# Kernel tuning notes

Measured on AMD Instinct MI355X. Metric: run time of the kernel, lower is better.

## Reference

```python
import jax, jax.numpy as jnp
import numpy as np

B_, L_, DM = 8, 1024, 256
DS, DC, EX = 16, 4, 2
DI = EX * DM            # d_inner = 512
DTR = max(1, DM // 16)  # dt_rank = 16


def setup_inputs() -> dict:
    key = jax.random.key(0)
    ks = iter(jax.random.split(key, 40))
    def n(shape, s=0.02):
        return jax.random.normal(next(ks), shape, jnp.float32) * s
    inp = {"x": jax.random.normal(next(ks), (B_, L_, DM), jnp.float32)}
    inp["norm_g"] = jnp.ones((DM,), jnp.float32)
    inp["norm_b"] = jnp.zeros((DM,), jnp.float32)
    for m in ("f", "b"):
        inp[f"inW_{m}"] = n((DM, 2 * DI))
        inp[f"convW_{m}"] = n((DI, DC))
        inp[f"convB_{m}"] = jnp.zeros((DI,), jnp.float32)
        inp[f"xW_{m}"] = n((DI, DTR + 2 * DS))
        inp[f"dtW_{m}"] = n((DTR, DI))
        inp[f"dtB_{m}"] = jnp.zeros((DI,), jnp.float32)
        # ALog init: log of [1..dState] repeated over dInner rows
        inp[f"ALog_{m}"] = jnp.log(jnp.tile(jnp.arange(1, DS + 1, dtype=jnp.float32), (DI, 1)))
        inp[f"Dp_{m}"] = jnp.ones((DI,), jnp.float32)
        inp[f"outW_{m}"] = n((DI, DM))
    inp["fusW"] = n((2 * DM, DM))
    inp["fusB"] = jnp.zeros((DM,), jnp.float32)
    return inp


def _dw_conv(x, w, b):
    # causal depthwise conv1d: x [B,L,DI], w [DI,DC] -> [B,L,DI]
    xc = jnp.transpose(x, (0, 2, 1))  # B,DI,L
    out = jax.lax.conv_general_dilated(
        xc, w[:, None, :], window_strides=(1,), padding=[(DC - 1, 0)],
        dimension_numbers=("NCH", "OIH", "NCH"), feature_group_count=DI)
    return jnp.transpose(out + b[:, None], (0, 2, 1))


def _ssm(x, xW, dtW, dtB, ALog, Dp):
    # x: [B,L,DI]
    A = -jnp.exp(ALog)                                   # [DI,DS]
    xdbl = x @ xW                                        # [B,L,DTR+2*DS]
    dlt, Bp, Cp = jnp.split(xdbl, [DTR, DTR + DS], axis=-1)
    delta = jax.nn.softplus(dlt @ dtW + dtB)             # [B,L,DI]
    dA = jnp.exp(delta[..., None] * A)                   # [B,L,DI,DS]
    dBx = (delta * x)[..., None] * Bp[:, :, None, :]     # [B,L,DI,DS]

    def step(h, t):
        a, bb, c = t
        h = a * h + bb                                   # [B,DI,DS]
        y = jnp.einsum('bdn,bn->bd', h, c)
        return h, y

    h0 = jnp.zeros((x.shape[0], DI, DS), x.dtype)
    _, ys = jax.lax.scan(step, h0, (jnp.moveaxis(dA, 1, 0),
                                    jnp.moveaxis(dBx, 1, 0),
                                    jnp.moveaxis(Cp, 1, 0)))
    return jnp.moveaxis(ys, 0, 1) + Dp * x               # [B,L,DI]


def _mamba(x, inW, convW, convB, xW, dtW, dtB, ALog, Dp, outW):
    xr = x @ inW                                         # [B,L,2*DI]
    xs, res = jnp.split(xr, 2, axis=-1)
    xs = jax.nn.silu(_dw_conv(xs, convW, convB))
    y = _ssm(xs, xW, dtW, dtB, ALog, Dp)
    return (y * jax.nn.silu(res)) @ outW                 # [B,L,DM]


def reference(x, norm_g, norm_b,
              inW_f, convW_f, convB_f, xW_f, dtW_f, dtB_f, ALog_f, Dp_f, outW_f,
              inW_b, convW_b, convB_b, xW_b, dtW_b, dtB_b, ALog_b, Dp_b, outW_b,
              fusW, fusB):
    # LayerNorm
    mu = x.mean(-1, keepdims=True)
    var = ((x - mu) ** 2).mean(-1, keepdims=True)
    xn = (x - mu) * jax.lax.rsqrt(var + 1e-5) * norm_g + norm_b
    # forward-direction Mamba
    xf = _mamba(xn, inW_f, convW_f, convB_f, xW_f, dtW_f, dtB_f, ALog_f, Dp_f, outW_f)
    # backward-direction Mamba (flip along time)
    xb = _mamba(jnp.flip(xn, 1), inW_b, convW_b, convB_b, xW_b, dtW_b, dtB_b, ALog_b, Dp_b, outW_b)
    xb = jnp.flip(xb, 1)
    fused = jnp.concatenate([xf, xb], axis=-1) @ fusW + fusB
    return x + fused  # dropout is identity in eval
```

## Files before the change

### kernel.cpp

```cpp
#include <hip/hip_runtime.h>
#include <cmath>

typedef __bf16 bf16x8 __attribute__((ext_vector_type(8)));
typedef __bf16 bf16x4 __attribute__((ext_vector_type(4)));
typedef float  f32x4  __attribute__((ext_vector_type(4)));
typedef float  f32x2  __attribute__((ext_vector_type(2)));

#define B_  8
#define L_  1024
#define DM  256
#define DI  512
#define DS  16
#define DTR 16
#define M_  (B_*L_)
#define NC  32
#define CT  32

__device__ inline float softplus_f(float z){
  return (z > 20.f) ? z : __logf(1.f + __expf(z));
}
__device__ inline float silu_f(float z){
  return z / (1.f + __expf(-z));
}

__device__ inline int flag_from_x(const void* x){
  const unsigned short* u = (const unsigned short*)x;
  int lane = threadIdx.x & 63;
  unsigned short v = u[2*lane];
  int e = (v >> 7) & 0xFF;
  unsigned long long m = __ballot(e >= 160 || e < 96);
  return __popcll(m) > 16;
}

struct PrepJob { const void* src; void* dst; int rows; int cols; int f32out; };
struct PrepArgs { PrepJob j[26]; int nj; };
struct TJob { const void* src; __bf16* dst; int R; int C; };
struct TArgs { TJob j[3]; int ntiles[3]; int nj; int ntot; };

__global__ __launch_bounds__(256) void wprep_k(TArgs ta, PrepArgs a, const void* xsrc){
  const int f = flag_from_x(xsrc);
  const int tid = threadIdx.x;
  if ((int)blockIdx.x < ta.ntot){
    __shared__ float tile[64][65];
    int bid = blockIdx.x;
    int jj = 0;
    while (jj < ta.nj-1 && bid >= ta.ntiles[jj]) { bid -= ta.ntiles[jj]; jj++; }
    const TJob J = ta.j[jj];
    const int tpr = J.C >> 6;
    const int tr = bid / tpr, tc = bid - tr*tpr;
    const int r0 = tr*64, c0 = tc*64;
    #pragma unroll
    for (int i=0;i<16;i++){
      int idx = i*256 + tid;
      int r = idx >> 6, c = idx & 63;
      long off = (long)(r0+r)*J.C + c0 + c;
      tile[r][c] = f ? ((const float*)J.src)[off] : (float)((const __bf16*)J.src)[off];
    }
    __syncthreads();
    #pragma unroll
    for (int i=0;i<16;i++){
      int idx = i*256 + tid;
      int c = idx >> 6, r = idx & 63;
      J.dst[(long)(c0+c)*J.R + r0 + r] = (__bf16)tile[r][c];
    }
  } else {
    int e = (blockIdx.x - ta.ntot)*256 + tid;
    #pragma unroll 1
    for (int jj=0; jj<a.nj; jj++){
      int sz = a.j[jj].rows * a.j[jj].cols;
      if (e < sz){
        int cols = a.j[jj].cols;
        int r = e / cols, c = e - r*cols;
        float v = f ? ((const float*)a.j[jj].src)[e] : (float)((const __bf16*)a.j[jj].src)[e];
        if (a.j[jj].f32out) ((float*)a.j[jj].dst)[c*a.j[jj].rows + r] = v;
        else ((__bf16*)a.j[jj].dst)[(long)c*a.j[jj].rows + r] = (__bf16)v;
        return;
      }
      e -= sz;
    }
  }
}

__global__ __launch_bounds__(256) void lnw_k(
    const void* x, const __bf16* g, const __bf16* bb, __bf16* xn,
    const __bf16* fusWt, const __bf16* outWr0, const __bf16* outWr1,
    __bf16* BtC0, __bf16* BtC1)
{
  const int bx = blockIdx.x;
  const int tid = threadIdx.x;
  const int lane = tid & 63;
  const int wid = tid >> 6;

  if (bx < M_/4){
    const int f = flag_from_x(x);
    long row = (long)bx*4 + wid;
    long base = row*DM + lane*4;
    float v0,v1,v2,v3;
    if (f){ f32x4 xv = *(const f32x4*)((const float*)x + base);
            v0=xv[0]; v1=xv[1]; v2=xv[2]; v3=xv[3]; }
    else  { bf16x4 xv = *(const bf16x4*)((const __bf16*)x + base);
            v0=(float)xv[0]; v1=(float)xv[1]; v2=(float)xv[2]; v3=(float)xv[3]; }
    float s = v0+v1+v2+v3;
    float q = v0*v0+v1*v1+v2*v2+v3*v3;
    #pragma unroll
    for (int off=32; off>0; off>>=1){ s += __shfl_xor(s,off); q += __shfl_xor(q,off); }
    float mu = s*(1.f/DM), var = q*(1.f/DM)-mu*mu;
    float rs = rsqrtf(var+1e-5f);
    bf16x4 gv = *(const bf16x4*)(g + lane*4);
    bf16x4 bv = *(const bf16x4*)(bb + lane*4);
    bf16x4 o;
    o[0]=(__bf16)((v0-mu)*rs*(float)gv[0]+(float)bv[0]);
    o[1]=(__bf16)((v1-mu)*rs*(float)gv[1]+(float)bv[1]);
    o[2]=(__bf16)((v2-mu)*rs*(float)gv[2]+(float)bv[2]);
    o[3]=(__bf16)((v3-mu)*rs*(float)gv[3]+(float)bv[3]);
    *(bf16x4*)(xn + base) = o;
  } else {
    int b2 = bx - M_/4;
    int wz  = b2 >> 5;
    int rem = b2 & 31;
    int gx = rem & 3, gy = rem >> 2;
    const __bf16* A  = fusWt + wz*DM;
    const __bf16* Bt = wz ? outWr1 : outWr0;
    __bf16* C = wz ? BtC1 : BtC0;
    const int mBase = (gx*4 + wid)*16;
    const int nBase = gy*64;
    const int lm = lane & 15;
    const int kq = (lane >> 4)*8;
    long aoff = (long)(mBase+lm)*(2*DM) + kq;
    long boff[4];
    #pragma unroll
    for (int j=0;j<4;j++) boff[j] = (long)(nBase+j*16+lm)*DM + kq;
    f32x4 acc[4] = {};
    #pragma unroll
    for (int k0=0;k0<DM;k0+=32){
      bf16x8 af = *(const bf16x8*)(A + aoff + k0);
      bf16x8 bfr[4];
      #pragma unroll
      for (int j=0;j<4;j++) bfr[j] = *(const bf16x8*)(Bt + boff[j] + k0);
      #pragma unroll
      for (int j=0;j<4;j++)
        acc[j] = __builtin_amdgcn_mfma_f32_16x16x32_bf16(af, bfr[j], acc[j], 0,0,0);
    }
    #pragma unroll
    for (int rr=0;rr<4;rr++){
      int r = mBase + (lane>>4)*4 + rr;
      #pragma unroll
      for (int j=0;j<4;j++){
        int c = nBase + j*16 + lm;
        C[(long)r*DI + c] = (__bf16)acc[j][rr];
      }
    }
  }
}

template<int BM,int BN,int KK>
__global__ __launch_bounds__(256) void gemm_in_k(
    const __bf16* A, const __bf16* B0, const __bf16* B1,
    __bf16* xz0, __bf16* xz1, __bf16* res0, __bf16* res1,
    int lda, int ldb)
{
  constexpr int TM = BM/2, TN = BN/2;
  constexpr int WMT = TM/16, WNT = TN/16;
  constexpr int LA = BM/64, LB = BN/64;

  const int dir = blockIdx.z;
  const __bf16* Bt = dir ? B1 : B0;
  __bf16* xz  = dir ? xz1 : xz0;
  __bf16* res = dir ? res1 : res0;
  const int tid  = threadIdx.x;
  const int lane = tid & 63;
  const int wid  = tid >> 6;
  const int wm = wid & 1;
  const int wn = wid >> 1;
  const int mBase = blockIdx.x * BM;
  const int nBase = blockIdx.y * BN;
  const int lm = lane & 15;
  const int kq = (lane >> 4) * 8;

  __shared__ __bf16 As[BM*32];
  __shared__ __bf16 Bs[BN*32];

  const __bf16* aS[LA];
  const __bf16* bS[LB];
  {
    int colk = (tid & 3) * 8;
    #pragma unroll
    for (int ld=0; ld<LA; ld++){
      int r = mBase + ld*64 + (tid >> 2);
      if (dir==1){ int b = r >> 10, t = r & (L_-1); r = (b<<10) + (L_-1-t); }
      aS[ld] = A + (long)r*lda + colk;
    }
    #pragma unroll
    for (int ld=0; ld<LB; ld++){
      int r = nBase + ld*64 + (tid >> 2);
      bS[ld] = Bt + (long)r*ldb + colk;
    }
  }

  f32x4 acc[WMT][WNT] = {};
  for (int k0=0; k0<KK; k0+=32){
    #pragma unroll
    for (int ld=0; ld<LA; ld++)
      __builtin_amdgcn_global_load_lds(
        (const __attribute__((address_space(1))) void*)(aS[ld] + k0),
        (__attribute__((address_space(3))) void*)(&As[ld*2048 + tid*8]), 16, 0, 0);
    #pragma unroll
    for (int ld=0; ld<LB; ld++)
      __builtin_amdgcn_global_load_lds(
        (const __attribute__((address_space(1))) void*)(bS[ld] + k0),
        (__attribute__((address_space(3))) void*)(&Bs[ld*2048 + tid*8]), 16, 0, 0);
    __syncthreads();
    bf16x8 af[WMT], bfr[WNT];
    #pragma unroll
    for (int i=0;i<WMT;i++) af[i]  = *(const bf16x8*)&As[(wm*TM + i*16 + lm)*32 + kq];
    #pragma unroll
    for (int j=0;j<WNT;j++) bfr[j] = *(const bf16x8*)&Bs[(wn*TN + j*16 + lm)*32 + kq];
    #pragma unroll
    for (int i=0;i<WMT;i++)
      #pragma unroll
      for (int j=0;j<WNT;j++)
        acc[i][j] = __builtin_amdgcn_mfma_f32_16x16x32_bf16(af[i], bfr[j], acc[i][j], 0,0,0);
    __syncthreads();
  }

  #pragma unroll
  for (int i=0;i<WMT;i++){
    #pragma unroll
    for (int rr=0;rr<4;rr++){
      int r = mBase + wm*TM + i*16 + (lane>>4)*4 + rr;
      #pragma unroll
      for (int j=0;j<WNT;j++){
        int c = nBase + wn*TN + j*16 + lm;
        float v = acc[i][j][rr];
        if (c < DI) xz[(long)r*DI + c] = (__bf16)v;
        else        res[(long)r*DI + (c-DI)] = (__bf16)v;
      }
    }
  }
}

template<int BM,int BN,int KK>
__global__ __launch_bounds__(256) void gemm_fin_k(
    const __bf16* Af, const __bf16* Ab,
    const __bf16* Bt0, const __bf16* Bt1,
    void* Cout, const __bf16* bias, const void* resid)
{
  constexpr int TM = BM/2, TN = BN/2;
  constexpr int WMT = TM/16, WNT = TN/16;
  constexpr int LA = BM/64, LB = BN/64;

  const int of = flag_from_x(resid);
  const int tid  = threadIdx.x;
  const int lane = tid & 63;
  const int wid  = tid >> 6;
  const int wm = wid & 1;
  const int wn = wid >> 1;
  const int mBase = blockIdx.x * BM;
  const int nBase = blockIdx.y * BN;
  const int lm = lane & 15;
  const int kq = (lane >> 4) * 8;

  __shared__ __bf16 As[BM*32];
  __shared__ __bf16 Bs[BN*32];

  f32x4 acc[WMT][WNT] = {};
  #pragma unroll 1
  for (int dd=0; dd<2; dd++){
    const __bf16* A  = dd ? Ab  : Af;
    const __bf16* Bt = dd ? Bt1 : Bt0;
    const __bf16* aS[LA];
    const __bf16* bS[LB];
    {
      int colk = (tid & 3) * 8;
      #pragma unroll
      for (int ld=0; ld<LA; ld++){
        int r = mBase + ld*64 + (tid >> 2);
        if (dd==1){ int b = r >> 10, t = r & (L_-1); r = (b<<10) + (L_-1-t); }
        aS[ld] = A + (long)r*DI + colk;
      }
      #pragma unroll
      for (int ld=0; ld<LB; ld++){
        int r = nBase + ld*64 + (tid >> 2);
        bS[ld] = Bt + (long)r*DI + colk;
      }
    }
    for (int k0=0; k0<KK; k0+=32){
      #pragma unroll
      for (int ld=0; ld<LA; ld++)
        __builtin_amdgcn_global_load_lds(
          (const __attribute__((address_space(1))) void*)(aS[ld] + k0),
          (__attribute__((address_space(3))) void*)(&As[ld*2048 + tid*8]), 16, 0, 0);
      #pragma unroll
      for (int ld=0; ld<LB; ld++)
        __builtin_amdgcn_global_load_lds(
          (const __attribute__((address_space(1))) void*)(bS[ld] + k0),
          (__attribute__((address_space(3))) void*)(&Bs[ld*2048 + tid*8]), 16, 0, 0);
      __syncthreads();
      bf16x8 af[WMT], bfr[WNT];
      #pragma unroll
      for (int i=0;i<WMT;i++) af[i]  = *(const bf16x8*)&As[(wm*TM + i*16 + lm)*32 + kq];
      #pragma unroll
      for (int j=0;j<WNT;j++) bfr[j] = *(const bf16x8*)&Bs[(wn*TN + j*16 + lm)*32 + kq];
      #pragma unroll
      for (int i=0;i<WMT;i++)
        #pragma unroll
        for (int j=0;j<WNT;j++)
          acc[i][j] = __builtin_amdgcn_mfma_f32_16x16x32_bf16(af[i], bfr[j], acc[i][j], 0,0,0);
      __syncthreads();
    }
  }

  #pragma unroll
  for (int i=0;i<WMT;i++){
    #pragma unroll
    for (int rr=0;rr<4;rr++){
      int r = mBase + wm*TM + i*16 + (lane>>4)*4 + rr;
      #pragma unroll
      for (int j=0;j<WNT;j++){
        int c = nBase + wn*TN + j*16 + lm;
        float v = acc[i][j][rr];
        float rsd = of ? ((const float*)resid)[(long)r*DM + c]
                       : (float)((const __bf16*)resid)[(long)r*DM + c];
        v += (float)bias[c] + rsd;
        if (of) ((float*)Cout)[(long)r*DM + c] = v;
        else    ((__bf16*)Cout)[(long)r*DM + c] = (__bf16)v;
      }
    }
  }
}

__global__ __launch_bounds__(512) void scanA_k(
    const __bf16* xz0, const __bf16* xz1,
    const float* cw0, const float* cw1,
    const __bf16* cb0, const __bf16* cb1,
    const __bf16* xW0, const __bf16* xW1,
    const float* dw0, const float* dw1,
    const __bf16* dtB0, const __bf16* dtB1,
    const float* ALf0, const float* ALf1,
    float* hend, float* sumd)
{
  const int dir = blockIdx.z;
  const __bf16* xz  = dir ? xz1 : xz0;
  const float*  cw  = dir ? cw1 : cw0;
  const __bf16* cb  = dir ? cb1 : cb0;
  const __bf16* xWt = dir ? xW1 : xW0;
  const float*  dw  = dir ? dw1 : dw0;
  const __bf16* dtB = dir ? dtB1 : dtB0;
  const float*  ALf = dir ? ALf1 : ALf0;

  const int b   = blockIdx.y;
  const int c   = blockIdx.x;
  const int tid = threadIdx.x;
  const int lane = tid & 63;
  const int wid  = tid >> 6;
  const int d   = tid;
  const int db  = dir*8 + b;
  const long row0 = (long)b*L_ + c*CT;

  __shared__ __bf16 xs_s[CT*DI];
  __shared__ float  sX[CT][48];

  {
    const float c0 = cw[0*DI+d], c1 = cw[1*DI+d], c2 = cw[2*DI+d], c3 = cw[3*DI+d];
    const float cbv = (float)cb[d];
    int gt0 = c*CT;
    float xm3 = (gt0-3 >= 0) ? (float)xz[(row0-3)*DI + d] : 0.f;
    float xm2 = (gt0-2 >= 0) ? (float)xz[(row0-2)*DI + d] : 0.f;
    float xm1 = (gt0-1 >= 0) ? (float)xz[(row0-1)*DI + d] : 0.f;
    #pragma unroll 8
    for (int t=0;t<CT;t++){
      float xt = (float)xz[(row0+t)*DI + d];
      float a = cbv;
      a += xm3*c0; a += xm2*c1; a += xm1*c2; a += xt*c3;
      float sv = silu_f(a);
      *(__bf16*)((char*)xs_s + t*1024 + ((2*d) ^ ((t&7)<<4))) = (__bf16)sv;
      xm3 = xm2; xm2 = xm1; xm1 = xt;
    }
  }
  __syncthreads();

  if (wid < 6){
    const int mb = (wid & 1) * 16;
    const int nb = (wid >> 1) * 16;
    const int lm = lane & 15;
    const int kq = (lane >> 4) * 8;
    const int row = mb + lm;
    const char* abase = (const char*)xs_s + row*1024;
    const int rsw = (row&7)<<4;
    const __bf16* Bt = xWt + (long)(nb + lm)*DI + kq;
    f32x4 acc = {};
    #pragma unroll
    for (int k0=0;k0<DI;k0+=32){
      bf16x8 af  = *(const bf16x8*)(abase + (((kq + k0)*2) ^ rsw));
      bf16x8 bfr = *(const bf16x8*)(Bt + k0);
      acc = __builtin_amdgcn_mfma_f32_16x16x32_bf16(af, bfr, acc, 0,0,0);
    }
    #pragma unroll
    for (int rr=0;rr<4;rr++){
      int r = mb + (lane>>4)*4 + rr;
      sX[r][nb + lm] = acc[rr];
    }
  }

  f32x2 dw2[8];
  { const f32x4* p = (const f32x4*)(dw + d*DTR);
    #pragma unroll
    for (int q=0;q<4;q++){ f32x4 v=p[q];
      dw2[q*2]   = f32x2{v[0],v[1]};
      dw2[q*2+1] = f32x2{v[2],v[3]}; } }
  float A[16];
  { const f32x4* p = (const f32x4*)(ALf + d*DS);
    #pragma unroll
    for (int q=0;q<4;q++){ f32x4 v=p[q];
      A[q*4]=-__expf(v[0]); A[q*4+1]=-__expf(v[1]); A[q*4+2]=-__expf(v[2]); A[q*4+3]=-__expf(v[3]); } }
  bool pow_ok = true;
  #pragma unroll
  for (int n=0;n<16;n++) pow_ok = pow_ok && (fabsf(A[n] + (float)(n+1)) < 0.003f*(n+1));
  const float dtbv = (float)dtB[d];

  f32x2 h2[8];
  #pragma unroll
  for (int i=0;i<8;i++) h2[i] = f32x2{0.f,0.f};
  float sdelta = 0.f;
  __syncthreads();

  if (pow_ok){
    #pragma unroll 2
    for (int t=0;t<CT;t++){
      f32x2 z2 = f32x2{dtbv, 0.f};
      #pragma unroll
      for (int i=0;i<8;i++){
        f32x2 qv = *(const f32x2*)&sX[t][i*2];
        z2 += qv*dw2[i];
      }
      float delta = softplus_f(z2[0]+z2[1]);
      sdelta += delta;
      float xv = (float)*(const __bf16*)((const char*)xs_s + t*1024 + ((2*d) ^ ((t&7)<<4)));
      float dx = delta*xv;
      f32x2 dx2 = f32x2{dx, dx};
      float e1 = __expf(-delta), e2v = e1*e1;
      f32x2 e22 = f32x2{e2v, e2v};
      f32x2 pw = f32x2{e1, e2v};
      #pragma unroll
      for (int i=0;i<8;i++){
        f32x2 Bv = *(const f32x2*)&sX[t][16+i*2];
        h2[i] = pw*h2[i] + dx2*Bv;
        pw = pw*e22;
      }
    }
  } else {
    #pragma unroll 2
    for (int t=0;t<CT;t++){
      f32x2 z2 = f32x2{dtbv, 0.f};
      #pragma unroll
      for (int i=0;i<8;i++){
        f32x2 qv = *(const f32x2*)&sX[t][i*2];
        z2 += qv*dw2[i];
      }
      float delta = softplus_f(z2[0]+z2[1]);
      sdelta += delta;
      float xv = (float)*(const __bf16*)((const char*)xs_s + t*1024 + ((2*d) ^ ((t&7)<<4)));
      float dx = delta*xv;
      #pragma unroll
      for (int i=0;i<8;i++){
        f32x2 Bv = *(const f32x2*)&sX[t][16+i*2];
        f32x2 pw = f32x2{__expf(delta*A[i*2]), __expf(delta*A[i*2+1])};
        h2[i] = pw*h2[i] + f32x2{dx,dx}*Bv;
      }
    }
  }

  long hb = (((long)db*NC + c)*DI + d)*16;
  f32x4* hp = (f32x4*)(hend + hb);
  #pragma unroll
  for (int q=0;q<4;q++){
    f32x4 v; v[0]=h2[q*2][0]; v[1]=h2[q*2][1]; v[2]=h2[q*2+1][0]; v[3]=h2[q*2+1][1];
    hp[q]=v;
  }
  sumd[((long)db*NC + c)*DI + d] = sdelta;
}

__global__ __launch_bounds__(256) void scanB_k(
    const float* ALf0, const float* ALf1,
    const float* hend, const float* sumd, float* Hbuf)
{
  int gid = blockIdx.x*256 + threadIdx.x;
  int n  = gid & 15;
  int d  = (gid>>4) & 511;
  int db = gid >> 13;
  const float* ALf = (db>=8) ? ALf1 : ALf0;
  float A_dn = -__expf(ALf[d*DS + n]);
  const long base0 = (((long)db*NC)*DI + d)*16 + n;
  const long cstr  = (long)DI*16;
  const long sbase = (long)db*NC*DI + d;
  float he[NC], Sv[NC];
  #pragma unroll
  for (int c=0;c<NC;c++) he[c] = hend[base0 + c*cstr];
  #pragma unroll
  for (int c=0;c<NC;c++) Sv[c] = sumd[sbase + c*DI];
  float H = 0.f;
  #pragma unroll
  for (int c=0;c<NC;c++){
    Hbuf[base0 + c*cstr] = H;
    H = he[c] + __expf(A_dn*Sv[c])*H;
  }
}

__global__ __launch_bounds__(512) void scanC_k(
    const __bf16* xz0, const __bf16* xz1,
    const float* cw0, const float* cw1,
    const __bf16* cb0, const __bf16* cb1,
    const __bf16* xW0, const __bf16* xW1,
    __bf16* res0, __bf16* res1,
    const float* dw0, const float* dw1,
    const __bf16* dtB0, const __bf16* dtB1,
    const float* ALf0, const float* ALf1,
    const __bf16* Dp0, const __bf16* Dp1,
    const float* Hbuf)
{
  const int dir = blockIdx.z;
  const __bf16* xz  = dir ? xz1 : xz0;
  const float*  cw  = dir ? cw1 : cw0;
  const __bf16* cb  = dir ? cb1 : cb0;
  const __bf16* xWt = dir ? xW1 : xW0;
  __bf16*       res = dir ? res1 : res0;
  const float*  dw  = dir ? dw1 : dw0;
  const __bf16* dtB = dir ? dtB1 : dtB0;
  const float*  ALf = dir ? ALf1 : ALf0;
  const __bf16* Dp  = dir ? Dp1 : Dp0;

  const int b   = blockIdx.y;
  const int c   = blockIdx.x;
  const int tid = threadIdx.x;
  const int lane = tid & 63;
  const int wid  = tid >> 6;
  const int d   = tid;
  const int db  = dir*8 + b;
  const long row0 = (long)b*L_ + c*CT;

  __shared__ __bf16 xs_s[CT*DI];
  __shared__ float  sX[CT][48];

  {
    const float c0 = cw[0*DI+d], c1 = cw[1*DI+d], c2 = cw[2*DI+d], c3 = cw[3*DI+d];
    const float cbv = (float)cb[d];
    int gt0 = c*CT;
    float xm3 = (gt0-3 >= 0) ? (float)xz[(row0-3)*DI + d] : 0.f;
    float xm2 = (gt0-2 >= 0) ? (float)xz[(row0-2)*DI + d] : 0.f;
    float xm1 = (gt0-1 >= 0) ? (float)xz[(row0-1)*DI + d] : 0.f;
    #pragma unroll 8
    for (int t=0;t<CT;t++){
      float xt = (float)xz[(row0+t)*DI + d];
      float a = cbv;
      a += xm3*c0; a += xm2*c1; a += xm1*c2; a += xt*c3;
      float sv = silu_f(a);
      *(__bf16*)((char*)xs_s + t*1024 + ((2*d) ^ ((t&7)<<4))) = (__bf16)sv;
      xm3 = xm2; xm2 = xm1; xm1 = xt;
    }
  }
  __syncthreads();

  if (wid < 6){
    const int mb = (wid & 1) * 16;
    const int nb = (wid >> 1) * 16;
    const int lm = lane & 15;
    const int kq = (lane >> 4) * 8;
    const int row = mb + lm;
    const char* abase = (const char*)xs_s + row*1024;
    const int rsw = (row&7)<<4;
    const __bf16* Bt = xWt + (long)(nb + lm)*DI + kq;
    f32x4 acc = {};
    #pragma unroll
    for (int k0=0;k0<DI;k0+=32){
      bf16x8 af  = *(const bf16x8*)(abase + (((kq + k0)*2) ^ rsw));
      bf16x8 bfr = *(const bf16x8*)(Bt + k0);
      acc = __builtin_amdgcn_mfma_f32_16x16x32_bf16(af, bfr, acc, 0,0,0);
    }
    #pragma unroll
    for (int rr=0;rr<4;rr++){
      int r = mb + (lane>>4)*4 + rr;
      sX[r][nb + lm] = acc[rr];
    }
  }

  f32x2 dw2[8];
  { const f32x4* p = (const f32x4*)(dw + d*DTR);
    #pragma unroll
    for (int q=0;q<4;q++){ f32x4 v=p[q];
      dw2[q*2]   = f32x2{v[0],v[1]};
      dw2[q*2+1] = f32x2{v[2],v[3]}; } }
  float A[16];
  { const f32x4* p = (const f32x4*)(ALf + d*DS);
    #pragma unroll
    for (int q=0;q<4;q++){ f32x4 v=p[q];
      A[q*4]=-__expf(v[0]); A[q*4+1]=-__expf(v[1]); A[q*4+2]=-__expf(v[2]); A[q*4+3]=-__expf(v[3]); } }
  bool pow_ok = true;
  #pragma unroll
  for (int n=0;n<16;n++) pow_ok = pow_ok && (fabsf(A[n] + (float)(n+1)) < 0.003f*(n+1));
  const float dtbv = (float)dtB[d];

  f32x2 h2[8];
  { long hb = (((long)db*NC + c)*DI + d)*16;
    const f32x4* p = (const f32x4*)(Hbuf + hb);
    #pragma unroll
    for (int q=0;q<4;q++){ f32x4 v = p[q];
      h2[q*2]   = f32x2{v[0],v[1]};
      h2[q*2+1] = f32x2{v[2],v[3]}; } }
  const float Dpv = (float)Dp[d];
  __syncthreads();

  if (pow_ok){
    #pragma unroll 2
    for (int t=0;t<CT;t++){
      long row = row0 + t;
      f32x2 z2 = f32x2{dtbv, 0.f};
      #pragma unroll
      for (int i=0;i<8;i++){
        f32x2 qv = *(const f32x2*)&sX[t][i*2];
        z2 += qv*dw2[i];
      }
      float delta = softplus_f(z2[0]+z2[1]);
      float xv = (float)*(const __bf16*)((const char*)xs_s + t*1024 + ((2*d) ^ ((t&7)<<4)));
      float dx = delta*xv;
      f32x2 dx2 = f32x2{dx, dx};
      float e1 = __expf(-delta), e2v = e1*e1;
      f32x2 e22 = f32x2{e2v, e2v};
      f32x2 pw = f32x2{e1, e2v};
      f32x2 p2 = f32x2{0.f, 0.f};
      #pragma unroll
      for (int i=0;i<8;i++){
        f32x2 Bv = *(const f32x2*)&sX[t][16+i*2];
        f32x2 Cv = *(const f32x2*)&sX[t][32+i*2];
        h2[i] = pw*h2[i] + dx2*Bv;
        p2 += h2[i]*Cv;
        pw = pw*e22;
      }
      float yv = p2[0] + p2[1] + Dpv*xv;
      float rv = (float)res[row*DI + d];
      res[row*DI + d] = (__bf16)(yv * silu_f(rv));
    }
  } else {
    #pragma unroll 2
    for (int t=0;t<CT;t++){
      long row = row0 + t;
      f32x2 z2 = f32x2{dtbv, 0.f};
      #pragma unroll
      for (int i=0;i<8;i++){
        f32x2 qv = *(const f32x2*)&sX[t][i*2];
        z2 += qv*dw2[i];
      }
      float delta = softplus_f(z2[0]+z2[1]);
      float xv = (float)*(const __bf16*)((const char*)xs_s + t*1024 + ((2*d) ^ ((t&7)<<4)));
      float dx = delta*xv;
      f32x2 p2 = f32x2{0.f, 0.f};
      #pragma unroll
      for (int i=0;i<8;i++){
        f32x2 Bv = *(const f32x2*)&sX[t][16+i*2];
        f32x2 Cv = *(const f32x2*)&sX[t][32+i*2];
        f32x2 pw = f32x2{__expf(delta*A[i*2]), __expf(delta*A[i*2+1])};
        h2[i] = pw*h2[i] + f32x2{dx,dx}*Bv;
        p2 += h2[i]*Cv;
      }
      float yv = p2[0] + p2[1] + Dpv*xv;
      float rv = (float)res[row*DI + d];
      res[row*DI + d] = (__bf16)(yv * silu_f(rv));
    }
  }
}

extern "C" void kernel_launch(void* const* d_in, const int* in_sizes, int n_in,
                              void* d_out, int out_size, void* d_ws, size_t ws_size,
                              hipStream_t stream)
{
  const size_t MB = 1u<<20;
  if (ws_size < 160*MB) return;

  char* w = (char*)d_ws;
  __bf16* xz[2]  = {(__bf16*)(w + 0),      (__bf16*)(w + 8*MB)};
  __bf16* res[2] = {(__bf16*)(w + 16*MB),  (__bf16*)(w + 24*MB)};
  __bf16* xn     = (__bf16*)(w + 48*MB);

  char* wp = w + 52*MB;
  auto carve = [&](size_t bytes)->void*{
    void* p = wp;
    wp += (bytes + 255) & ~(size_t)255;
    return p;
  };
  __bf16 *inWt[2], *xWt[2], *outWr[2], *BtC[2];
  float *dtWt[2], *convWt[2];
  for (int m=0;m<2;m++){
    inWt[m]   = (__bf16*)carve((size_t)(2*DI)*DM*2);
    xWt[m]    = (__bf16*)carve((size_t)48*DI*2);
    outWr[m]  = (__bf16*)carve((size_t)DI*DM*2);
    BtC[m]    = (__bf16*)carve((size_t)DM*DI*2);
    dtWt[m]   = (float*)carve((size_t)DI*DTR*4);
    convWt[m] = (float*)carve((size_t)4*DI*4);
  }
  __bf16* fusWt = (__bf16*)carve((size_t)DM*(2*DM)*2);
  float* ALf[2] = {(float*)carve((size_t)DI*DS*4), (float*)carve((size_t)DI*DS*4)};

  char* cp = w + 57*MB;
  auto carve2 = [&](size_t elems)->__bf16*{
    __bf16* p = (__bf16*)cp;
    cp += (elems*2 + 255) & ~(size_t)255;
    return p;
  };
  __bf16* ngc = carve2(DM);
  __bf16* nbc = carve2(DM);
  __bf16 *convBc[2], *dtBc[2], *Dpc[2];
  for (int m=0;m<2;m++){
    convBc[m] = carve2(DI);
    dtBc[m]   = carve2(DI);
    Dpc[m]    = carve2(DI);
  }
  __bf16* fusBc = carve2(DM);

  float* hend = (float*)(w + 90*MB);
  float* sumd = (float*)(w + 124*MB);
  float* Hbuf = (float*)(w + 127*MB);

  PrepArgs pa;
  int ji = 0;
  size_t tot = 0;
  auto addj = [&](const void* s, void* dst, int rows, int cols, int f32o){
    pa.j[ji++] = {s, dst, rows, cols, f32o};
    tot += (size_t)rows*cols;
  };
  for (int m=0;m<2;m++){
    int base = 3 + m*9;
    addj(d_in[base+3], xWt[m],   DI,  48,   0);
    addj(d_in[base+8], outWr[m], 1,   DI*DM,0);
    addj(d_in[base+4], dtWt[m],  DTR, DI,   1);
    addj(d_in[base+1], convWt[m],DI,  4,    1);
    addj(d_in[base+2], convBc[m],1, DI, 0);
    addj(d_in[base+5], dtBc[m],  1, DI, 0);
    addj(d_in[base+6], (void*)ALf[m], 1, DI*DS, 1);
    addj(d_in[base+7], Dpc[m],   1, DI, 0);
  }
  addj(d_in[1],  ngc, 1, DM, 0);
  addj(d_in[2],  nbc, 1, DM, 0);
  addj(d_in[22], fusBc, 1, DM, 0);
  pa.nj = ji;

  TArgs ta;
  ta.j[0] = { d_in[3],  inWt[0], DM,   2*DI }; ta.ntiles[0] = (DM/64)*((2*DI)/64);
  ta.j[1] = { d_in[12], inWt[1], DM,   2*DI }; ta.ntiles[1] = (DM/64)*((2*DI)/64);
  ta.j[2] = { d_in[21], fusWt,   2*DM, DM   }; ta.ntiles[2] = ((2*DM)/64)*(DM/64);
  ta.nj = 3;
  ta.ntot = ta.ntiles[0]+ta.ntiles[1]+ta.ntiles[2];
  int prepBlocks = (int)((tot+255)/256);
  wprep_k<<<ta.ntot + prepBlocks, 256, 0, stream>>>(ta, pa, d_in[0]);

  lnw_k<<<M_/4 + 64, 256, 0, stream>>>(
      d_in[0], ngc, nbc, xn, fusWt, outWr[0], outWr[1], BtC[0], BtC[1]);

  gemm_in_k<128,128,256><<<dim3(M_/128, (2*DI)/128, 2), 256, 0, stream>>>(
      xn, inWt[0], inWt[1], xz[0], xz[1], res[0], res[1], DM, DM);

  scanA_k<<<dim3(NC, B_, 2), 512, 0, stream>>>(
      xz[0], xz[1], convWt[0], convWt[1], convBc[0], convBc[1],
      xWt[0], xWt[1], dtWt[0], dtWt[1],
      dtBc[0], dtBc[1], ALf[0], ALf[1], hend, sumd);
  scanB_k<<<131072/256, 256, 0, stream>>>(ALf[0], ALf[1], hend, sumd, Hbuf);
  scanC_k<<<dim3(NC, B_, 2), 512, 0, stream>>>(
      xz[0], xz[1], convWt[0], convWt[1], convBc[0], convBc[1],
      xWt[0], xWt[1], res[0], res[1],
      dtWt[0], dtWt[1], dtBc[0], dtBc[1], ALf[0], ALf[1], Dpc[0], Dpc[1], Hbuf);

  gemm_fin_k<64,64,DI><<<dim3(M_/64, DM/64, 1), 256, 0, stream>>>(
      res[0], res[1], BtC[0], BtC[1], d_out, fusBc, d_in[0]);
}
```

Before: 236.4 us.

## Halve scan chunk length to double chunk count and trim per-thread registers

The time chunk size drops from 32 to 16 steps, so there are 64 chunks per sequence. This doubles the number of blocks in the chunked scan kernels and halves each block's serial recurrence. The MFMA projection tiles are reduced to a single 16-row tile. The per-thread A array is dropped and recomputed from ALog inside the fallback paths, which saves registers. In exchange, the cross-chunk carry kernel now runs a sequential chain twice as long, processed in groups of 16 to bound registers, and more carry state is written to workspace, so the buffers are moved.

```diff
diff --git a/kernel.cpp b/kernel.cpp
--- a/kernel.cpp
+++ b/kernel.cpp
@@ -13,8 +13,8 @@
 #define DS  16
 #define DTR 16
 #define M_  (B_*L_)
-#define NC  32
-#define CT  32
+#define NC  64
+#define CT  16
 
 __device__ inline float softplus_f(float z){
   return (z > 20.f) ? z : __logf(1.f + __expf(z));
@@ -358,7 +358,7 @@
   const long row0 = (long)b*L_ + c*CT;
 
   __shared__ __bf16 xs_s[CT*DI];
-  __shared__ float  sX[CT][48];
+  __shared__ float  sX[CT][32];
 
   {
     const float c0 = cw[0*DI+d], c1 = cw[1*DI+d], c2 = cw[2*DI+d], c3 = cw[3*DI+d];
@@ -367,7 +367,7 @@
     float xm3 = (gt0-3 >= 0) ? (float)xz[(row0-3)*DI + d] : 0.f;
     float xm2 = (gt0-2 >= 0) ? (float)xz[(row0-2)*DI + d] : 0.f;
     float xm1 = (gt0-1 >= 0) ? (float)xz[(row0-1)*DI + d] : 0.f;
-    #pragma unroll 8
+    #pragma unroll
     for (int t=0;t<CT;t++){
       float xt = (float)xz[(row0+t)*DI + d];
       float a = cbv;
@@ -379,12 +379,11 @@
   }
   __syncthreads();
 
-  if (wid < 6){
-    const int mb = (wid & 1) * 16;
-    const int nb = (wid >> 1) * 16;
+  if (wid < 2){
+    const int nb = wid * 16;
     const int lm = lane & 15;
     const int kq = (lane >> 4) * 8;
-    const int row = mb + lm;
+    const int row = lm;
     const char* abase = (const char*)xs_s + row*1024;
     const int rsw = (row&7)<<4;
     const __bf16* Bt = xWt + (long)(nb + lm)*DI + kq;
@@ -397,7 +396,7 @@
     }
     #pragma unroll
     for (int rr=0;rr<4;rr++){
-      int r = mb + (lane>>4)*4 + rr;
+      int r = (lane>>4)*4 + rr;
       sX[r][nb + lm] = acc[rr];
     }
   }
@@ -408,14 +407,12 @@
     for (int q=0;q<4;q++){ f32x4 v=p[q];
       dw2[q*2]   = f32x2{v[0],v[1]};
       dw2[q*2+1] = f32x2{v[2],v[3]}; } }
-  float A[16];
-  { const f32x4* p = (const f32x4*)(ALf + d*DS);
-    #pragma unroll
-    for (int q=0;q<4;q++){ f32x4 v=p[q];
-      A[q*4]=-__expf(v[0]); A[q*4+1]=-__expf(v[1]); A[q*4+2]=-__expf(v[2]); A[q*4+3]=-__expf(v[3]); } }
   bool pow_ok = true;
-  #pragma unroll
-  for (int n=0;n<16;n++) pow_ok = pow_ok && (fabsf(A[n] + (float)(n+1)) < 0.003f*(n+1));
+  #pragma unroll 1
+  for (int n=0;n<16;n++){
+    float An = -__expf(ALf[d*DS + n]);
+    pow_ok = pow_ok && (fabsf(An + (float)(n+1)) < 0.003f*(n+1));
+  }
   const float dtbv = (float)dtB[d];
 
   f32x2 h2[8];
@@ -463,8 +460,9 @@
       float dx = delta*xv;
       #pragma unroll
       for (int i=0;i<8;i++){
+        f32x2 A2 = f32x2{-__expf(ALf[d*DS+i*2]), -__expf(ALf[d*DS+i*2+1])};
         f32x2 Bv = *(const f32x2*)&sX[t][16+i*2];
-        f32x2 pw = f32x2{__expf(delta*A[i*2]), __expf(delta*A[i*2+1])};
+        f32x2 pw = f32x2{__expf(delta*A2[0]), __expf(delta*A2[1])};
         h2[i] = pw*h2[i] + f32x2{dx,dx}*Bv;
       }
     }
@@ -493,16 +491,20 @@
   const long base0 = (((long)db*NC)*DI + d)*16 + n;
   const long cstr  = (long)DI*16;
   const long sbase = (long)db*NC*DI + d;
-  float he[NC], Sv[NC];
-  #pragma unroll
-  for (int c=0;c<NC;c++) he[c] = hend[base0 + c*cstr];
-  #pragma unroll
-  for (int c=0;c<NC;c++) Sv[c] = sumd[sbase + c*DI];
   float H = 0.f;
-  #pragma unroll
-  for (int c=0;c<NC;c++){
-    Hbuf[base0 + c*cstr] = H;
-    H = he[c] + __expf(A_dn*Sv[c])*H;
+  #pragma unroll 1
+  for (int g=0; g<NC/16; g++){
+    float he[16], Sv[16];
+    #pragma unroll
+    for (int k=0;k<16;k++){
+      he[k] = hend[base0 + (long)(g*16+k)*cstr];
+      Sv[k] = sumd[sbase + (long)(g*16+k)*DI];
+    }
+    #pragma unroll
+    for (int k=0;k<16;k++){
+      Hbuf[base0 + (long)(g*16+k)*cstr] = H;
+      H = he[k] + __expf(A_dn*Sv[k])*H;
+    }
   }
 }
 
@@ -548,7 +550,7 @@
     float xm3 = (gt0-3 >= 0) ? (float)xz[(row0-3)*DI + d] : 0.f;
     float xm2 = (gt0-2 >= 0) ? (float)xz[(row0-2)*DI + d] : 0.f;
     float xm1 = (gt0-1 >= 0) ? (float)xz[(row0-1)*DI + d] : 0.f;
-    #pragma unroll 8
+    #pragma unroll
     for (int t=0;t<CT;t++){
       float xt = (float)xz[(row0+t)*DI + d];
       float a = cbv;
@@ -560,12 +562,11 @@
   }
   __syncthreads();
 
-  if (wid < 6){
-    const int mb = (wid & 1) * 16;
-    const int nb = (wid >> 1) * 16;
+  if (wid < 3){
+    const int nb = wid * 16;
     const int lm = lane & 15;
     const int kq = (lane >> 4) * 8;
-    const int row = mb + lm;
+    const int row = lm;
     const char* abase = (const char*)xs_s + row*1024;
     const int rsw = (row&7)<<4;
     const __bf16* Bt = xWt + (long)(nb + lm)*DI + kq;
@@ -578,7 +579,7 @@
     }
     #pragma unroll
     for (int rr=0;rr<4;rr++){
-      int r = mb + (lane>>4)*4 + rr;
+      int r = (lane>>4)*4 + rr;
       sX[r][nb + lm] = acc[rr];
     }
   }
@@ -589,14 +590,12 @@
     for (int q=0;q<4;q++){ f32x4 v=p[q];
       dw2[q*2]   = f32x2{v[0],v[1]};
       dw2[q*2+1] = f32x2{v[2],v[3]}; } }
-  float A[16];
-  { const f32x4* p = (const f32x4*)(ALf + d*DS);
-    #pragma unroll
-    for (int q=0;q<4;q++){ f32x4 v=p[q];
-      A[q*4]=-__expf(v[0]); A[q*4+1]=-__expf(v[1]); A[q*4+2]=-__expf(v[2]); A[q*4+3]=-__expf(v[3]); } }
   bool pow_ok = true;
-  #pragma unroll
-  for (int n=0;n<16;n++) pow_ok = pow_ok && (fabsf(A[n] + (float)(n+1)) < 0.003f*(n+1));
+  #pragma unroll 1
+  for (int n=0;n<16;n++){
+    float An = -__expf(ALf[d*DS + n]);
+    pow_ok = pow_ok && (fabsf(An + (float)(n+1)) < 0.003f*(n+1));
+  }
   const float dtbv = (float)dtB[d];
 
   f32x2 h2[8];
@@ -655,9 +654,10 @@
       f32x2 p2 = f32x2{0.f, 0.f};
       #pragma unroll
       for (int i=0;i<8;i++){
+        f32x2 A2 = f32x2{-__expf(ALf[d*DS+i*2]), -__expf(ALf[d*DS+i*2+1])};
         f32x2 Bv = *(const f32x2*)&sX[t][16+i*2];
         f32x2 Cv = *(const f32x2*)&sX[t][32+i*2];
-        f32x2 pw = f32x2{__expf(delta*A[i*2]), __expf(delta*A[i*2+1])};
+        f32x2 pw = f32x2{__expf(delta*A2[0]), __expf(delta*A2[1])};
         h2[i] = pw*h2[i] + f32x2{dx,dx}*Bv;
         p2 += h2[i]*Cv;
       }
@@ -716,8 +716,8 @@
   __bf16* fusBc = carve2(DM);
 
   float* hend = (float*)(w + 90*MB);
-  float* sumd = (float*)(w + 124*MB);
-  float* Hbuf = (float*)(w + 127*MB);
+  float* Hbuf = (float*)(w + 122*MB);
+  float* sumd = (float*)(w + 154*MB);
 
   PrepArgs pa;
   int ji = 0;
```

New measurement: 266.2 us. 1.13x slower.

## Halve scan chunk length and interleave two independent chunks per block

Applied to the files above, without the earlier changes.

The chunked selective scan now uses 64 chunks of 16 timesteps. Each block handles two adjacent chunks and runs their recurrences interleaved, so every thread carries two independent dependency chains, which halves the serial chain length and adds instruction-level parallelism. The first scan pass also skips computing the C projection it never used, leaving 4 MFMA waves instead of 6. In exchange the cross-chunk scanB pass handles twice as many chunk carries, the hend/Hbuf workspace doubles, and register pressure rises from holding two state vectors.

```diff
diff --git a/kernel.cpp b/kernel.cpp
--- a/kernel.cpp
+++ b/kernel.cpp
@@ -13,8 +13,9 @@
 #define DS  16
 #define DTR 16
 #define M_  (B_*L_)
-#define NC  32
-#define CT  32
+#define NC  64
+#define CT  16
+#define CTB 32
 
 __device__ inline float softplus_f(float z){
   return (z > 20.f) ? z : __logf(1.f + __expf(z));
@@ -349,29 +350,30 @@
   const float*  ALf = dir ? ALf1 : ALf0;
 
   const int b   = blockIdx.y;
-  const int c   = blockIdx.x;
+  const int g   = blockIdx.x;
+  const int c0  = g*2, c1 = g*2+1;
   const int tid = threadIdx.x;
   const int lane = tid & 63;
   const int wid  = tid >> 6;
   const int d   = tid;
   const int db  = dir*8 + b;
-  const long row0 = (long)b*L_ + c*CT;
-
-  __shared__ __bf16 xs_s[CT*DI];
-  __shared__ float  sX[CT][48];
+  const long row0 = (long)b*L_ + (long)c0*CT;
+
+  __shared__ __bf16 xs_s[CTB*DI];
+  __shared__ float  sX[CTB][32];
 
   {
-    const float c0 = cw[0*DI+d], c1 = cw[1*DI+d], c2 = cw[2*DI+d], c3 = cw[3*DI+d];
+    const float q0 = cw[0*DI+d], q1 = cw[1*DI+d], q2 = cw[2*DI+d], q3 = cw[3*DI+d];
     const float cbv = (float)cb[d];
-    int gt0 = c*CT;
+    int gt0 = c0*CT;
     float xm3 = (gt0-3 >= 0) ? (float)xz[(row0-3)*DI + d] : 0.f;
     float xm2 = (gt0-2 >= 0) ? (float)xz[(row0-2)*DI + d] : 0.f;
     float xm1 = (gt0-1 >= 0) ? (float)xz[(row0-1)*DI + d] : 0.f;
     #pragma unroll 8
-    for (int t=0;t<CT;t++){
+    for (int t=0;t<CTB;t++){
       float xt = (float)xz[(row0+t)*DI + d];
       float a = cbv;
-      a += xm3*c0; a += xm2*c1; a += xm1*c2; a += xt*c3;
+      a += xm3*q0; a += xm2*q1; a += xm1*q2; a += xt*q3;
       float sv = silu_f(a);
       *(__bf16*)((char*)xs_s + t*1024 + ((2*d) ^ ((t&7)<<4))) = (__bf16)sv;
       xm3 = xm2; xm2 = xm1; xm1 = xt;
@@ -379,7 +381,7 @@
   }
   __syncthreads();
 
-  if (wid < 6){
+  if (wid < 4){
     const int mb = (wid & 1) * 16;
     const int nb = (wid >> 1) * 16;
     const int lm = lane & 15;
@@ -418,66 +420,84 @@
   for (int n=0;n<16;n++) pow_ok = pow_ok && (fabsf(A[n] + (float)(n+1)) < 0.003f*(n+1));
   const float dtbv = (float)dtB[d];
 
-  f32x2 h2[8];
+  f32x2 hA[8], hB[8];
   #pragma unroll
-  for (int i=0;i<8;i++) h2[i] = f32x2{0.f,0.f};
-  float sdelta = 0.f;
+  for (int i=0;i<8;i++){ hA[i] = f32x2{0.f,0.f}; hB[i] = f32x2{0.f,0.f}; }
+  float sdA = 0.f, sdB = 0.f;
   __syncthreads();
 
   if (pow_ok){
     #pragma unroll 2
     for (int t=0;t<CT;t++){
-      f32x2 z2 = f32x2{dtbv, 0.f};
+      f32x2 zA = f32x2{dtbv, 0.f}, zB = f32x2{dtbv, 0.f};
       #pragma unroll
       for (int i=0;i<8;i++){
-        f32x2 qv = *(const f32x2*)&sX[t][i*2];
-        z2 += qv*dw2[i];
-      }
-      float delta = softplus_f(z2[0]+z2[1]);
-      sdelta += delta;
-      float xv = (float)*(const __bf16*)((const char*)xs_s + t*1024 + ((2*d) ^ ((t&7)<<4)));
-      float dx = delta*xv;
-      f32x2 dx2 = f32x2{dx, dx};
-      float e1 = __expf(-delta), e2v = e1*e1;
-      f32x2 e22 = f32x2{e2v, e2v};
-      f32x2 pw = f32x2{e1, e2v};
+        zA += (*(const f32x2*)&sX[t][i*2])      * dw2[i];
+        zB += (*(const f32x2*)&sX[CT+t][i*2])   * dw2[i];
+      }
+      float dlA = softplus_f(zA[0]+zA[1]);
+      float dlB = softplus_f(zB[0]+zB[1]);
+      sdA += dlA; sdB += dlB;
+      const int swz = (2*d) ^ ((t&7)<<4);
+      float xvA = (float)*(const __bf16*)((const char*)xs_s + t*1024 + swz);
+      float xvB = (float)*(const __bf16*)((const char*)xs_s + (CT+t)*1024 + swz);
+      float dxA = dlA*xvA, dxB = dlB*xvB;
+      float e1A = __expf(-dlA), e2A = e1A*e1A;
+      float e1B = __expf(-dlB), e2B = e1B*e1B;
+      f32x2 pwA = f32x2{e1A, e2A}, pwB = f32x2{e1B, e2B};
+      f32x2 e22A = f32x2{e2A, e2A}, e22B = f32x2{e2B, e2B};
       #pragma unroll
       for (int i=0;i<8;i++){
-        f32x2 Bv = *(const f32x2*)&sX[t][16+i*2];
-        h2[i] = pw*h2[i] + dx2*Bv;
-        pw = pw*e22;
+        f32x2 BvA = *(const f32x2*)&sX[t][16+i*2];
+        f32x2 BvB = *(const f32x2*)&sX[CT+t][16+i*2];
+        hA[i] = pwA*hA[i] + f32x2{dxA,dxA}*BvA;
+        hB[i] = pwB*hB[i] + f32x2{dxB,dxB}*BvB;
+        pwA = pwA*e22A; pwB = pwB*e22B;
       }
     }
   } else {
     #pragma unroll 2
     for (int t=0;t<CT;t++){
-      f32x2 z2 = f32x2{dtbv, 0.f};
+      f32x2 zA = f32x2{dtbv, 0.f}, zB = f32x2{dtbv, 0.f};
       #pragma unroll
       for (int i=0;i<8;i++){
-        f32x2 qv = *(const f32x2*)&sX[t][i*2];
-        z2 += qv*dw2[i];
-      }
-      float delta = softplus_f(z2[0]+z2[1]);
-      sdelta += delta;
-      float xv = (float)*(const __bf16*)((const char*)xs_s + t*1024 + ((2*d) ^ ((t&7)<<4)));
-      float dx = delta*xv;
+        zA += (*(const f32x2*)&sX[t][i*2])    * dw2[i];
+        zB += (*(const f32x2*)&sX[CT+t][i*2]) * dw2[i];
+      }
+      float dlA = softplus_f(zA[0]+zA[1]);
+      float dlB = softplus_f(zB[0]+zB[1]);
+      sdA += dlA; sdB += dlB;
+      const int swz = (2*d) ^ ((t&7)<<4);
+      float xvA = (float)*(const __bf16*)((const char*)xs_s + t*1024 + swz);
+      float xvB = (float)*(const __bf16*)((const char*)xs_s + (CT+t)*1024 + swz);
+      float dxA = dlA*xvA, dxB = dlB*xvB;
       #pragma unroll
       for (int i=0;i<8;i++){
-        f32x2 Bv = *(const f32x2*)&sX[t][16+i*2];
-        f32x2 pw = f32x2{__expf(delta*A[i*2]), __expf(delta*A[i*2+1])};
-        h2[i] = pw*h2[i] + f32x2{dx,dx}*Bv;
-      }
-    }
-  }
-
-  long hb = (((long)db*NC + c)*DI + d)*16;
-  f32x4* hp = (f32x4*)(hend + hb);
-  #pragma unroll
-  for (int q=0;q<4;q++){
-    f32x4 v; v[0]=h2[q*2][0]; v[1]=h2[q*2][1]; v[2]=h2[q*2+1][0]; v[3]=h2[q*2+1][1];
-    hp[q]=v;
-  }
-  sumd[((long)db*NC + c)*DI + d] = sdelta;
+        f32x2 BvA = *(const f32x2*)&sX[t][16+i*2];
+        f32x2 BvB = *(const f32x2*)&sX[CT+t][16+i*2];
+        f32x2 pwA = f32x2{__expf(dlA*A[i*2]), __expf(dlA*A[i*2+1])};
+        f32x2 pwB = f32x2{__expf(dlB*A[i*2]), __expf(dlB*A[i*2+1])};
+        hA[i] = pwA*hA[i] + f32x2{dxA,dxA}*BvA;
+        hB[i] = pwB*hB[i] + f32x2{dxB,dxB}*BvB;
+      }
+    }
+  }
+
+  {
+    long hbA = (((long)db*NC + c0)*DI + d)*16;
+    long hbB = (((long)db*NC + c1)*DI + d)*16;
+    f32x4* hpA = (f32x4*)(hend + hbA);
+    f32x4* hpB = (f32x4*)(hend + hbB);
+    #pragma unroll
+    for (int q=0;q<4;q++){
+      f32x4 v; v[0]=hA[q*2][0]; v[1]=hA[q*2][1]; v[2]=hA[q*2+1][0]; v[3]=hA[q*2+1][1];
+      hpA[q]=v;
+      f32x4 u; u[0]=hB[q*2][0]; u[1]=hB[q*2][1]; u[2]=hB[q*2+1][0]; u[3]=hB[q*2+1][1];
+      hpB[q]=u;
+    }
+    sumd[((long)db*NC + c0)*DI + d] = sdA;
+    sumd[((long)db*NC + c1)*DI + d] = sdB;
+  }
 }
 
 __global__ __launch_bounds__(256) void scanB_k(
@@ -493,16 +513,20 @@
   const long base0 = (((long)db*NC)*DI + d)*16 + n;
   const long cstr  = (long)DI*16;
   const long sbase = (long)db*NC*DI + d;
-  float he[NC], Sv[NC];
-  #pragma unroll
-  for (int c=0;c<NC;c++) he[c] = hend[base0 + c*cstr];
-  #pragma unroll
-  for (int c=0;c<NC;c++) Sv[c] = sumd[sbase + c*DI];
   float H = 0.f;
-  #pragma unroll
-  for (int c=0;c<NC;c++){
-    Hbuf[base0 + c*cstr] = H;
-    H = he[c] + __expf(A_dn*Sv[c])*H;
+  #pragma unroll 1
+  for (int g=0; g<NC/16; g++){
+    float he[16], Sv[16];
+    #pragma unroll
+    for (int k=0;k<16;k++){
+      he[k] = hend[base0 + (long)(g*16+k)*cstr];
+      Sv[k] = sumd[sbase + (long)(g*16+k)*DI];
+    }
+    #pragma unroll
+    for (int k=0;k<16;k++){
+      Hbuf[base0 + (long)(g*16+k)*cstr] = H;
+      H = he[k] + __expf(A_dn*Sv[k])*H;
+    }
   }
 }
 
@@ -530,29 +554,30 @@
   const __bf16* Dp  = dir ? Dp1 : Dp0;
 
   const int b   = blockIdx.y;
-  const int c   = blockIdx.x;
+  const int g   = blockIdx.x;
+  const int c0  = g*2, c1 = g*2+1;
   const int tid = threadIdx.x;
   const int lane = tid & 63;
   const int wid  = tid >> 6;
   const int d   = tid;
   const int db  = dir*8 + b;
-  const long row0 = (long)b*L_ + c*CT;
-
-  __shared__ __bf16 xs_s[CT*DI];
-  __shared__ float  sX[CT][48];
+  const long row0 = (long)b*L_ + (long)c0*CT;
+
+  __shared__ __bf16 xs_s[CTB*DI];
+  __shared__ float  sX[CTB][48];
 
   {
-    const float c0 = cw[0*DI+d], c1 = cw[1*DI+d], c2 = cw[2*DI+d], c3 = cw[3*DI+d];
+    const float q0 = cw[0*DI+d], q1 = cw[1*DI+d], q2 = cw[2*DI+d], q3 = cw[3*DI+d];
     const float cbv = (float)cb[d];
-    int gt0 = c*CT;
+    int gt0 = c0*CT;
     float xm3 = (gt0-3 >= 0) ? (float)xz[(row0-3)*DI + d] : 0.f;
     float xm2 = (gt0-2 >= 0) ? (float)xz[(row0-2)*DI + d] : 0.f;
     float xm1 = (gt0-1 >= 0) ? (float)xz[(row0-1)*DI + d] : 0.f;
     #pragma unroll 8
-    for (int t=0;t<CT;t++){
+    for (int t=0;t<CTB;t++){
       float xt = (float)xz[(row0+t)*DI + d];
       float a = cbv;
-      a += xm3*c0; a += xm2*c1; a += xm1*c2; a += xt*c3;
+      a += xm3*q0; a += xm2*q1; a += xm1*q2; a += xt*q3;
       float sv = silu_f(a);
       *(__bf16*)((char*)xs_s + t*1024 + ((2*d) ^ ((t&7)<<4))) = (__bf16)sv;
       xm3 = xm2; xm2 = xm1; xm1 = xt;
@@ -599,71 +624,99 @@
   for (int n=0;n<16;n++) pow_ok = pow_ok && (fabsf(A[n] + (float)(n+1)) < 0.003f*(n+1));
   const float dtbv = (float)dtB[d];
 
-  f32x2 h2[8];
-  { long hb = (((long)db*NC + c)*DI + d)*16;
-    const f32x4* p = (const f32x4*)(Hbuf + hb);
-    #pragma unroll
-    for (int q=0;q<4;q++){ f32x4 v = p[q];
-      h2[q*2]   = f32x2{v[0],v[1]};
-      h2[q*2+1] = f32x2{v[2],v[3]}; } }
+  f32x2 hA[8], hB[8];
+  { long hbA = (((long)db*NC + c0)*DI + d)*16;
+    long hbB = (((long)db*NC + c1)*DI + d)*16;
+    const f32x4* pA = (const f32x4*)(Hbuf + hbA);
+    const f32x4* pB = (const f32x4*)(Hbuf + hbB);
+    #pragma unroll
+    for (int q=0;q<4;q++){
+      f32x4 v = pA[q];
+      hA[q*2]   = f32x2{v[0],v[1]};
+      hA[q*2+1] = f32x2{v[2],v[3]};
+      f32x4 u = pB[q];
+      hB[q*2]   = f32x2{u[0],u[1]};
+      hB[q*2+1] = f32x2{u[2],u[3]};
+    } }
   const float Dpv = (float)Dp[d];
   __syncthreads();
 
   if (pow_ok){
     #pragma unroll 2
     for (int t=0;t<CT;t++){
-      long row = row0 + t;
-      f32x2 z2 = f32x2{dtbv, 0.f};
+      f32x2 zA = f32x2{dtbv, 0.f}, zB = f32x2{dtbv, 0.f};
       #pragma unroll
       for (int i=0;i<8;i++){
-        f32x2 qv = *(const f32x2*)&sX[t][i*2];
-        z2 += qv*dw2[i];
-      }
-      float delta = softplus_f(z2[0]+z2[1]);
-      float xv = (float)*(const __bf16*)((const char*)xs_s + t*1024 + ((2*d) ^ ((t&7)<<4)));
-      float dx = delta*xv;
-      f32x2 dx2 = f32x2{dx, dx};
-      float e1 = __expf(-delta), e2v = e1*e1;
-      f32x2 e22 = f32x2{e2v, e2v};
-      f32x2 pw = f32x2{e1, e2v};
-      f32x2 p2 = f32x2{0.f, 0.f};
+        zA += (*(const f32x2*)&sX[t][i*2])    * dw2[i];
+        zB += (*(const f32x2*)&sX[CT+t][i*2]) * dw2[i];
+      }
+      float dlA = softplus_f(zA[0]+zA[1]);
+      float dlB = softplus_f(zB[0]+zB[1]);
+      const int swz = (2*d) ^ ((t&7)<<4);
+      float xvA = (float)*(const __bf16*)((const char*)xs_s + t*1024 + swz);
+      float xvB = (float)*(const __bf16*)((const char*)xs_s + (CT+t)*1024 + swz);
+      float dxA = dlA*xvA, dxB = dlB*xvB;
+      float e1A = __expf(-dlA), e2A = e1A*e1A;
+      float e1B = __expf(-dlB), e2B = e1B*e1B;
+      f32x2 pwA = f32x2{e1A, e2A}, pwB = f32x2{e1B, e2B};
+      f32x2 e22A = f32x2{e2A, e2A}, e22B = f32x2{e2B, e2B};
+      f32x2 p2A = f32x2{0.f,0.f}, p2B = f32x2{0.f,0.f};
       #pragma unroll
       for (int i=0;i<8;i++){
-        f32x2 Bv = *(const f32x2*)&sX[t][16+i*2];
-        f32x2 Cv = *(const f32x2*)&sX[t][32+i*2];
-        h2[i] = pw*h2[i] + dx2*Bv;
-        p2 += h2[i]*Cv;
-        pw = pw*e22;
-      }
-      float yv = p2[0] + p2[1] + Dpv*xv;
-      float rv = (float)res[row*DI + d];
-      res[row*DI + d] = (__bf16)(yv * silu_f(rv));
+        f32x2 BvA = *(const f32x2*)&sX[t][16+i*2];
+        f32x2 CvA = *(const f32x2*)&sX[t][32+i*2];
+        f32x2 BvB = *(const f32x2*)&sX[CT+t][16+i*2];
+        f32x2 CvB = *(const f32x2*)&sX[CT+t][32+i*2];
+        hA[i] = pwA*hA[i] + f32x2{dxA,dxA}*BvA;
+        p2A += hA[i]*CvA;
+        hB[i] = pwB*hB[i] + f32x2{dxB,dxB}*BvB;
+        p2B += hB[i]*CvB;
+        pwA = pwA*e22A; pwB = pwB*e22B;
+      }
+      float yA = p2A[0] + p2A[1] + Dpv*xvA;
+      float yB = p2B[0] + p2B[1] + Dpv*xvB;
+      long rowA = row0 + t, rowB = row0 + CT + t;
+      float rA = (float)res[rowA*DI + d];
+      float rB = (float)res[rowB*DI + d];
+      res[rowA*DI + d] = (__bf16)(yA * silu_f(rA));
+      res[rowB*DI + d] = (__bf16)(yB * silu_f(rB));
     }
   } else {
     #pragma unroll 2
     for (int t=0;t<CT;t++){
-      long row = row0 + t;
-      f32x2 z2 = f32x2{dtbv, 0.f};
+      f32x2 zA = f32x2{dtbv, 0.f}, zB = f32x2{dtbv, 0.f};
       #pragma unroll
       for (int i=0;i<8;i++){
-        f32x2 qv = *(const f32x2*)&sX[t][i*2];
-        z2 += qv*dw2[i];
-      }
-      float delta = softplus_f(z2[0]+z2[1]);
-      float xv = (float)*(const __bf16*)((const char*)xs_s + t*1024 + ((2*d) ^ ((t&7)<<4)));
-      float dx = delta*xv;
-      f32x2 p2 = f32x2{0.f, 0.f};
+        zA += (*(const f32x2*)&sX[t][i*2])    * dw2[i];
+        zB += (*(const f32x2*)&sX[CT+t][i*2]) * dw2[i];
+      }
+      float dlA = softplus_f(zA[0]+zA[1]);
+      float dlB = softplus_f(zB[0]+zB[1]);
+      const int swz = (2*d) ^ ((t&7)<<4);
+      float xvA = (float)*(const __bf16*)((const char*)xs_s + t*1024 + swz);
+      float xvB = (float)*(const __bf16*)((const char*)xs_s + (CT+t)*1024 + swz);
+      float dxA = dlA*xvA, dxB = dlB*xvB;
+      f32x2 p2A = f32x2{0.f,0.f}, p2B = f32x2{0.f,0.f};
       #pragma unroll
       for (int i=0;i<8;i++){
-        f32x2 Bv = *(const f32x2*)&sX[t][16+i*2];
-        f32x2 Cv = *(const f32x2*)&sX[t][32+i*2];
-        f32x2 pw = f32x2{__expf(delta*A[i*2]), __expf(delta*A[i*2+1])};
-        h2[i] = pw*h2[i] + f32x2{dx,dx}*Bv;
-        p2 += h2[i]*Cv;
-      }
-      float yv = p2[0] + p2[1] + Dpv*xv;
-      float rv = (float)res[row*DI + d];
-      res[row*DI + d] = (__bf16)(yv * silu_f(rv));
+        f32x2 BvA = *(const f32x2*)&sX[t][16+i*2];
+        f32x2 CvA = *(const f32x2*)&sX[t][32+i*2];
+        f32x2 BvB = *(const f32x2*)&sX[CT+t][16+i*2];
+        f32x2 CvB = *(const f32x2*)&sX[CT+t][32+i*2];
+        f32x2 pwA = f32x2{__expf(dlA*A[i*2]), __expf(dlA*A[i*2+1])};
+        f32x2 pwB = f32x2{__expf(dlB*A[i*2]), __expf(dlB*A[i*2+1])};
+        hA[i] = pwA*hA[i] + f32x2{dxA,dxA}*BvA;
+        p2A += hA[i]*CvA;
+        hB[i] = pwB*hB[i] + f32x2{dxB,dxB}*BvB;
+        p2B += hB[i]*CvB;
+      }
+      float yA = p2A[0] + p2A[1] + Dpv*xvA;
+      float yB = p2B[0] + p2B[1] + Dpv*xvB;
+      long rowA = row0 + t, rowB = row0 + CT + t;
+      float rA = (float)res[rowA*DI + d];
+      float rB = (float)res[rowB*DI + d];
+      res[rowA*DI + d] = (__bf16)(yA * silu_f(rA));
+      res[rowB*DI + d] = (__bf16)(yB * silu_f(rB));
     }
   }
 }
@@ -716,8 +769,8 @@
   __bf16* fusBc = carve2(DM);
 
   float* hend = (float*)(w + 90*MB);
-  float* sumd = (float*)(w + 124*MB);
-  float* Hbuf = (float*)(w + 127*MB);
+  float* Hbuf = (float*)(w + 122*MB);
+  float* sumd = (float*)(w + 154*MB);
 
   PrepArgs pa;
   int ji = 0;
@@ -757,12 +810,12 @@
   gemm_in_k<128,128,256><<<dim3(M_/128, (2*DI)/128, 2), 256, 0, stream>>>(
       xn, inWt[0], inWt[1], xz[0], xz[1], res[0], res[1], DM, DM);
 
-  scanA_k<<<dim3(NC, B_, 2), 512, 0, stream>>>(
+  scanA_k<<<dim3(NC/2, B_, 2), 512, 0, stream>>>(
       xz[0], xz[1], convWt[0], convWt[1], convBc[0], convBc[1],
       xWt[0], xWt[1], dtWt[0], dtWt[1],
       dtBc[0], dtBc[1], ALf[0], ALf[1], hend, sumd);
   scanB_k<<<131072/256, 256, 0, stream>>>(ALf[0], ALf[1], hend, sumd, Hbuf);
-  scanC_k<<<dim3(NC, B_, 2), 512, 0, stream>>>(
+  scanC_k<<<dim3(NC/2, B_, 2), 512, 0, stream>>>(
       xz[0], xz[1], convWt[0], convWt[1], convBc[0], convBc[1],
       xWt[0], xWt[1], res[0], res[1],
       dtWt[0], dtWt[1], dtBc[0], dtBc[1], ALf[0], ALf[1], Dpc[0], Dpc[1], Hbuf);
```

Result: slower. 274.0 us (+15.9%).
